# Performance work log

Hardware: AMD Instinct MI355X
Metric: run time of the kernel (lower is better)

## Reference

```python
import jax, jax.numpy as jnp
import numpy as np

H = 4096      # hidden_size
D = 1024      # mem_dim
A = 512       # attn_dim
B, LQ, TM = 4, 2048, 1500
EPS = 1e-5


def _layernorm(x, w, b):
    mu = jnp.mean(x, axis=-1, keepdims=True)
    var = jnp.var(x, axis=-1, keepdims=True)
    return (x - mu) * jax.lax.rsqrt(var + EPS) * w + b


def setup_inputs() -> dict:
    key = jax.random.key(0)
    ks = jax.random.split(key, 12)
    s = lambda fan_in: 1.0 / np.sqrt(fan_in)
    return {
        "hidden": jax.random.normal(ks[0], (B, LQ, H), jnp.float32),
        "mem": jax.random.normal(ks[1], (B, TM, D), jnp.float32),
        "mem_mask": jnp.zeros((B, TM), dtype=bool),
        "Wq": jax.random.uniform(ks[2], (H, A), jnp.float32, -s(H), s(H)),
        "bq": jnp.zeros((A,), jnp.float32),
        "Wk": jax.random.uniform(ks[3], (D, A), jnp.float32, -s(D), s(D)),
        "bk": jnp.zeros((A,), jnp.float32),
        "Wv": jax.random.uniform(ks[4], (D, A), jnp.float32, -s(D), s(D)),
        "bv": jnp.zeros((A,), jnp.float32),
        "Wo": jax.random.uniform(ks[5], (A, H), jnp.float32, -s(A), s(A)),
        "bo": jnp.zeros((H,), jnp.float32),
        "ln_in_w": jnp.ones((H,), jnp.float32),
        "ln_in_b": jnp.zeros((H,), jnp.float32),
        "ln_out_w": jnp.ones((H,), jnp.float32),
        "ln_out_b": jnp.zeros((H,), jnp.float32),
        "gate_logit": jnp.float32(-2.0),
    }


def reference(hidden, mem, mem_mask, Wq, bq, Wk, bk, Wv, bv, Wo, bo,
              ln_in_w, ln_in_b, ln_out_w, ln_out_b, gate_logit):
    h_norm = _layernorm(hidden, ln_in_w, ln_in_b)            # [B,LQ,H]
    Q = h_norm @ Wq + bq                                     # [B,LQ,A]
    K = mem @ Wk + bk                                        # [B,TM,A]
    V = mem @ Wv + bv                                        # [B,TM,A]
    scale = 1.0 / jnp.sqrt(jnp.float32(Q.shape[-1]))
    scores = jnp.einsum('bqa,bka->bqk', Q, K) * scale        # [B,LQ,TM]
    scores = jnp.where(mem_mask[:, None, :], jnp.float32(-1e30), scores)
    attn = jax.nn.softmax(scores, axis=-1)
    context = jnp.einsum('bqk,bka->bqa', attn, V)            # [B,LQ,A]
    context_h = context @ Wo + bo                            # [B,LQ,H]
    out_base = _layernorm(hidden + context_h, ln_out_w, ln_out_b)
    g = jax.nn.sigmoid(gate_logit)
    return hidden + g * (out_base - hidden)
```

## Files before the change

### kernel.cpp

```cpp
#include <hip/hip_runtime.h>
#include <cstdint>
#include <cstddef>

#define H_   4096
#define D_   1024
#define A_   512
#define B_   4
#define LQ_  2048
#define TM_  1500
#define TMP_ 1536
#define EPS_ 1e-5f

typedef __attribute__((ext_vector_type(8))) _Float16 half8;
typedef __attribute__((ext_vector_type(4))) _Float16 half4v;
typedef __attribute__((ext_vector_type(4))) float f32x4;

__device__ __forceinline__ void gload_lds16(void* g, void* l) {
  __builtin_amdgcn_global_load_lds((__attribute__((address_space(1))) void*)g,
                                   (__attribute__((address_space(3))) void*)l,
                                   16, 0, 0);
}

template <int OUTMODE>
__device__ __forceinline__ void gemm_tile(
    const _Float16* __restrict__ A, int lda,
    const _Float16* __restrict__ Bt, int ldb,
    const float* __restrict__ bias,
    void* __restrict__ C, int ldc,
    int Mvalid, int m0, int n0, int kbase, int kiters, float scale,
    _Float16* As, _Float16* Bs,
    const unsigned char* __restrict__ mrow, float* __restrict__ lsum, int nvalid) {
  const int tid = threadIdx.x;
  const int lane = tid & 63;
  const int wave = tid >> 6;

  f32x4 acc[4][4];
#pragma unroll
  for (int i = 0; i < 4; ++i)
#pragma unroll
    for (int jj = 0; jj < 4; ++jj) acc[i][jj] = (f32x4){0.f, 0.f, 0.f, 0.f};

  const _Float16* gA[2];
  const _Float16* gB[2];
  _Float16* lA[2];
  _Float16* lB[2];
#pragma unroll
  for (int i = 0; i < 2; ++i) {
    const int c = wave * 64 + lane + 256 * i;
    const int r = c >> 2;
    const int cs = c & 3;
    const int col = (cs ^ ((r >> 1) & 3)) * 8;
    int ra = m0 + r;
    if (ra >= Mvalid) ra = Mvalid - 1;
    gA[i] = A + (size_t)ra * lda + kbase + col;
    gB[i] = Bt + (size_t)(n0 + r) * ldb + kbase + col;
    lA[i] = As + wave * 512 + i * 2048;
    lB[i] = Bs + wave * 512 + i * 2048;
  }

  const int wm = (wave >> 1) * 64;
  const int wn = (wave & 1) * 64;
  const int rsub = lane & 15;
  const int j = lane >> 4;
  const int slot = j ^ ((rsub >> 1) & 3);

  for (int kt = 0; kt < kiters; ++kt) {
    const int ko = kt * 32;
#pragma unroll
    for (int i = 0; i < 2; ++i) {
      gload_lds16((void*)(gA[i] + ko), (void*)lA[i]);
      gload_lds16((void*)(gB[i] + ko), (void*)lB[i]);
    }
    __syncthreads();
    half8 af[4], bfr[4];
#pragma unroll
    for (int x = 0; x < 4; ++x) {
      af[x]  = *(const half8*)&As[(wm + x * 16 + rsub) * 32 + slot * 8];
      bfr[x] = *(const half8*)&Bs[(wn + x * 16 + rsub) * 32 + slot * 8];
    }
#pragma unroll
    for (int mi = 0; mi < 4; ++mi)
#pragma unroll
      for (int ni = 0; ni < 4; ++ni)
        acc[mi][ni] = __builtin_amdgcn_mfma_f32_16x16x32_f16(af[mi], bfr[ni], acc[mi][ni], 0, 0, 0);
    __syncthreads();
  }

  const int cn = n0 + wn + rsub;
  const int rm = m0 + wm + j * 4;

  if (OUTMODE == 3) {
    bool ok[4];
#pragma unroll
    for (int ni = 0; ni < 4; ++ni) {
      const int n = cn + ni * 16;
      const int nc = n < nvalid ? n : nvalid - 1;
      ok[ni] = (n < nvalid) && (mrow[nc] == 0);
    }
#pragma unroll
    for (int mi = 0; mi < 4; ++mi) {
#pragma unroll
      for (int r = 0; r < 4; ++r) {
        const int m = rm + mi * 16 + r;
        float rowsum = 0.f;
#pragma unroll
        for (int ni = 0; ni < 4; ++ni) {
          const int n = cn + ni * 16;
          const float e = ok[ni] ? __expf(acc[mi][ni][r] * scale) : 0.f;
          ((_Float16*)C)[(size_t)m * ldc + n] = (_Float16)e;
          rowsum += e;
        }
#pragma unroll
        for (int d = 1; d < 16; d <<= 1) rowsum += __shfl_xor(rowsum, d);
        if (rsub == 0) atomicAdd(&lsum[m], rowsum);
      }
    }
    return;
  }

  if (OUTMODE == 1) {
#pragma unroll
    for (int ni = 0; ni < 4; ++ni) {
      const int n = cn + ni * 16;
      const float bi = bias ? bias[n] : 0.f;
#pragma unroll
      for (int mi = 0; mi < 4; ++mi) {
        half4v pk;
#pragma unroll
        for (int r = 0; r < 4; ++r) pk[r] = (_Float16)(acc[mi][ni][r] * scale + bi);
        *(half4v*)&((_Float16*)C)[(size_t)n * ldc + rm + mi * 16] = pk;
      }
    }
    return;
  }

#pragma unroll
  for (int ni = 0; ni < 4; ++ni) {
    const int n = cn + ni * 16;
    const float bi = (OUTMODE == 0 && bias) ? bias[n] : 0.f;
#pragma unroll
    for (int mi = 0; mi < 4; ++mi) {
#pragma unroll
      for (int r = 0; r < 4; ++r) {
        const int m = rm + mi * 16 + r;
        const float v = acc[mi][ni][r] * scale + bi;
        if (OUTMODE == 0) ((_Float16*)C)[(size_t)m * ldc + n] = (_Float16)v;
        else ((float*)C)[(size_t)m * ldc + n] = v;
      }
    }
  }
}

template <int OUTMODE>
__global__ __launch_bounds__(256) void gemm_nt_kernel(
    const _Float16* __restrict__ Aall, size_t strideA, int lda,
    const _Float16* __restrict__ Btall, size_t strideB, int ldb,
    const float* __restrict__ bias,
    void* __restrict__ Call, size_t strideC, size_t strideS,
    int ldc, int Mvalid, int kiters, int nslices, int sliceK, float scale) {
  __shared__ __align__(16) _Float16 As[4096];
  __shared__ __align__(16) _Float16 Bs[4096];
  const int nx = gridDim.x, ny = gridDim.y;
  int id = (int)blockIdx.x + nx * ((int)blockIdx.y + ny * (int)blockIdx.z);
  const int tot = nx * ny * (int)gridDim.z;
  id = (id & 7) * (tot >> 3) + (id >> 3);
  const int bx = id % nx;
  const int by = (id / nx) % ny;
  const int bz = id / (nx * ny);
  const int batch = bz / nslices;
  const int slice = bz % nslices;
  const _Float16* A = Aall + (size_t)batch * strideA;
  const _Float16* Bt = Btall + (size_t)batch * strideB;
  char* C = (char*)Call + ((size_t)batch * strideC + (size_t)slice * strideS) *
                          (OUTMODE == 2 ? 4 : 2);
  gemm_tile<OUTMODE>(A, lda, Bt, ldb, bias, (void*)C, ldc, Mvalid,
                     by * 128, bx * 128, slice * sliceK, kiters,
                     scale, As, Bs, nullptr, nullptr, 0);
}

#define WO_NKH 16
__global__ __launch_bounds__(512, 1) void wo8_kernel(
    const _Float16* __restrict__ Ag,
    const _Float16* __restrict__ Bg,
    const float* __restrict__ bias,
    _Float16* __restrict__ Cg) {
  __shared__ __align__(16) _Float16 lds[65536];
  const int tid = threadIdx.x;
  const int lane = tid & 63;
  const int wave = tid >> 6;
  const int wr = wave >> 2;
  const int wc = wave & 3;
  int id = (int)blockIdx.x;
  id = (id & 7) * 64 + (id >> 3);
  const int by = id >> 4;
  const int bx = id & 15;
  const int m0 = by * 256, n0 = bx * 256;

  const _Float16* srcA[2];
  const _Float16* srcB[2];
  _Float16* dstA[2];
  _Float16* dstB[2];
#pragma unroll
  for (int p = 0; p < 2; ++p) {
    const int c = p * 512 + tid;
    const int r = c >> 2, cs = c & 3;
    const int col = (cs ^ ((r >> 1) & 3)) * 8;
    srcA[p] = Ag + (size_t)(m0 + r) * 512 + col;
    srcB[p] = Bg + (size_t)(n0 + r) * 512 + col;
    dstA[p] = lds + (p * 512 + wave * 64) * 8;
    dstB[p] = lds + 32768 + (p * 512 + wave * 64) * 8;
  }

  const int rsub = lane & 15;
  const int j = lane >> 4;
  const int sc_ = j ^ ((rsub >> 1) & 3);

  f32x4 acc[8][4];
#pragma unroll
  for (int i = 0; i < 8; ++i)
#pragma unroll
    for (int n = 0; n < 4; ++n) acc[i][n] = (f32x4){0.f, 0.f, 0.f, 0.f};

#pragma unroll
  for (int p = 0; p < 2; ++p) gload_lds16((void*)(srcA[p]), (void*)(dstA[p]));
#pragma unroll
  for (int p = 0; p < 2; ++p) gload_lds16((void*)(srcB[p]), (void*)(dstB[p]));
#pragma unroll
  for (int p = 0; p < 2; ++p) gload_lds16((void*)(srcA[p] + 32), (void*)(dstA[p] + 8192));
#pragma unroll
  for (int p = 0; p < 2; ++p) gload_lds16((void*)(srcB[p] + 32), (void*)(dstB[p] + 8192));
  asm volatile("s_waitcnt vmcnt(4)" ::: "memory");
  __builtin_amdgcn_s_barrier();

  half8 bf[4];
  for (int h = 0; h < WO_NKH; ++h) {
    const int sl = h & 3;
    const _Float16* Asl = lds + sl * 8192;
    const _Float16* Bsl = lds + 32768 + sl * 8192;
    if (h + 2 < WO_NKH) {
      const int s2 = (h + 2) & 3;
#pragma unroll
      for (int p = 0; p < 2; ++p)
        gload_lds16((void*)(srcA[p] + (h + 2) * 32), (void*)(dstA[p] + s2 * 8192));
    }
    half8 af[4];
#pragma unroll
    for (int x = 0; x < 4; ++x) {
      af[x] = *(const half8*)&Asl[(wr * 128 + x * 16 + rsub) * 32 + sc_ * 8];
      bf[x] = *(const half8*)&Bsl[(wc * 64 + x * 16 + rsub) * 32 + sc_ * 8];
    }
    __builtin_amdgcn_s_barrier();
    __builtin_amdgcn_s_setprio(1);
#pragma unroll
    for (int mi = 0; mi < 4; ++mi)
#pragma unroll
      for (int ni = 0; ni < 4; ++ni)
        acc[mi][ni] = __builtin_amdgcn_mfma_f32_16x16x32_f16(af[mi], bf[ni], acc[mi][ni], 0, 0, 0);
    __builtin_amdgcn_s_setprio(0);
    __builtin_amdgcn_s_barrier();
    if (h + 2 < WO_NKH) {
      const int s2 = (h + 2) & 3;
#pragma unroll
      for (int p = 0; p < 2; ++p)
        gload_lds16((void*)(srcB[p] + (h + 2) * 32), (void*)(dstB[p] + s2 * 8192));
    }
#pragma unroll
    for (int x = 0; x < 4; ++x)
      af[x] = *(const half8*)&Asl[(wr * 128 + 64 + x * 16 + rsub) * 32 + sc_ * 8];
    if (h < WO_NKH - 2) {
      asm volatile("s_waitcnt vmcnt(4)" ::: "memory");
    } else if (h == WO_NKH - 2) {
      asm volatile("s_waitcnt vmcnt(0)" ::: "memory");
    }
    __builtin_amdgcn_s_barrier();
    __builtin_amdgcn_s_setprio(1);
#pragma unroll
    for (int mi = 0; mi < 4; ++mi)
#pragma unroll
      for (int ni = 0; ni < 4; ++ni)
        acc[4 + mi][ni] = __builtin_amdgcn_mfma_f32_16x16x32_f16(af[mi], bf[ni], acc[4 + mi][ni], 0, 0, 0);
    __builtin_amdgcn_s_setprio(0);
    __builtin_amdgcn_s_barrier();
  }

  const int cn0 = n0 + wc * 64 + rsub;
  const int rm0 = m0 + wr * 128 + j * 4;
#pragma unroll
  for (int ni = 0; ni < 4; ++ni) {
    const int n = cn0 + ni * 16;
    const float bi = bias[n];
#pragma unroll
    for (int mh = 0; mh < 2; ++mh)
#pragma unroll
      for (int mi = 0; mi < 4; ++mi)
#pragma unroll
        for (int r = 0; r < 4; ++r) {
          const int m = rm0 + mh * 64 + mi * 16 + r;
          Cg[(size_t)m * 4096 + n] = (_Float16)(acc[mh * 4 + mi][ni][r] + bi);
        }
  }
}

__global__ __launch_bounds__(256) void scores_kernel(
    const _Float16* __restrict__ Qh, const _Float16* __restrict__ Kp,
    _Float16* __restrict__ sc, const unsigned char* __restrict__ mask,
    float* __restrict__ lsum) {
  __shared__ __align__(16) _Float16 As[4096];
  __shared__ __align__(16) _Float16 Bs[4096];
  const int nx = gridDim.x, ny = gridDim.y;
  int id = (int)blockIdx.x + nx * ((int)blockIdx.y + ny * (int)blockIdx.z);
  const int tot = nx * ny * (int)gridDim.z;
  id = (id & 7) * (tot >> 3) + (id >> 3);
  const int bx = id % nx;
  const int by = (id / nx) % ny;
  const int b = id / (nx * ny);
  gemm_tile<3>(Qh + (size_t)b * LQ_ * A_, A_, Kp + (size_t)b * TMP_ * A_, A_, nullptr,
               (void*)(sc + (size_t)b * LQ_ * TMP_), TMP_, LQ_,
               by * 128, bx * 128, 0, 16, 0.044194173824159216f,
               As, Bs, mask + (size_t)b * TM_, lsum + (size_t)b * LQ_, TM_);
}

__global__ __launch_bounds__(256) void qkv_kernel(
    const _Float16* __restrict__ hnorm, const _Float16* __restrict__ WqT,
    float* __restrict__ Qpart,
    const _Float16* __restrict__ memh, const _Float16* __restrict__ WkT,
    const float* __restrict__ bk, _Float16* __restrict__ Kp,
    const _Float16* __restrict__ WvT, const float* __restrict__ bv,
    _Float16* __restrict__ VT) {
  __shared__ __align__(16) _Float16 As[4096];
  __shared__ __align__(16) _Float16 Bs[4096];
  const int bid0 = blockIdx.x;
  if (bid0 < 512) {
    const int bid = ((bid0 & 7) << 6) | (bid0 >> 3);
    const int nb = bid & 3, mb = (bid >> 2) & 63, ks = bid >> 8;
    gemm_tile<2>(hnorm, H_, WqT, H_, nullptr,
                 (void*)(Qpart + (size_t)ks * 8192 * A_), A_,
                 8192, mb * 128, nb * 128, ks * 2048, 64, 1.f, As, Bs,
                 nullptr, nullptr, 0);
  } else if (bid0 < 704) {
    int t = bid0 - 512;
    t = (t & 7) * 24 + (t >> 3);
    const int nb = t & 3, mb = (t >> 2) % 12, b = t / 48;
    gemm_tile<0>(memh + (size_t)b * TM_ * D_, D_, WkT, D_, bk,
                 (void*)(Kp + (size_t)b * TMP_ * A_), A_,
                 TM_, mb * 128, nb * 128, 0, 32, 1.f, As, Bs,
                 nullptr, nullptr, 0);
  } else {
    int t = bid0 - 704;
    t = (t & 7) * 24 + (t >> 3);
    const int nb = t & 3, mb = (t >> 2) % 12, b = t / 48;
    gemm_tile<1>(memh + (size_t)b * TM_ * D_, D_, WvT, D_, bv,
                 (void*)(VT + (size_t)b * A_ * TMP_), TMP_,
                 TM_, mb * 128, nb * 128, 0, 32, 1.f, As, Bs,
                 nullptr, nullptr, 0);
  }
}

__global__ __launch_bounds__(256) void qreduce_kernel(
    const float* __restrict__ p, const float* __restrict__ bias,
    _Float16* __restrict__ out, float* __restrict__ lsum) {
  const int bid = blockIdx.x;
  if (bid >= 4096) {
    lsum[(bid - 4096) * 256 + threadIdx.x] = 0.f;
    return;
  }
  const size_t i = ((size_t)bid * 256 + threadIdx.x) * 4;
  const float4 a = *(const float4*)(p + i);
  const float4 b = *(const float4*)(p + (size_t)8192 * A_ + i);
  const float4 bi = *(const float4*)(bias + (i & (A_ - 1)));
  half4v o;
  o.x = (_Float16)(a.x + b.x + bi.x);
  o.y = (_Float16)(a.y + b.y + bi.y);
  o.z = (_Float16)(a.z + b.z + bi.z);
  o.w = (_Float16)(a.w + b.w + bi.w);
  *(half4v*)(out + i) = o;
}

__global__ __launch_bounds__(256) void areduce_kernel(
    const float* __restrict__ p, const float* __restrict__ lsum,
    _Float16* __restrict__ out) {
  const size_t S = (size_t)B_ * LQ_ * A_;
  const size_t i = ((size_t)blockIdx.x * 256 + threadIdx.x) * 4;
  const float4 a = *(const float4*)(p + i);
  const float4 b = *(const float4*)(p + S + i);
  const float4 c = *(const float4*)(p + 2 * S + i);
  const float inv = 1.f / lsum[i >> 9];
  half4v o;
  o.x = (_Float16)((a.x + b.x + c.x) * inv);
  o.y = (_Float16)((a.y + b.y + c.y) * inv);
  o.z = (_Float16)((a.z + b.z + c.z) * inv);
  o.w = (_Float16)((a.w + b.w + c.w) * inv);
  *(half4v*)(out + i) = o;
}

__global__ __launch_bounds__(256) void ln1_kernel(
    const float* __restrict__ hidden, const float* __restrict__ lnw,
    const float* __restrict__ lnb, _Float16* __restrict__ hnorm) {
  const int t = threadIdx.x;
  const int lane = t & 63;
  const int row = blockIdx.x * 4 + (t >> 6);
  const float* x = hidden + (size_t)row * H_;
  _Float16* y = hnorm + (size_t)row * H_;
  float4 v[16];
  float s = 0.f, ss = 0.f;
#pragma unroll
  for (int i = 0; i < 16; ++i) {
    v[i] = ((const float4*)x)[lane + 64 * i];
    s  += v[i].x + v[i].y + v[i].z + v[i].w;
    ss += v[i].x * v[i].x + v[i].y * v[i].y + v[i].z * v[i].z + v[i].w * v[i].w;
  }
#pragma unroll
  for (int off = 32; off; off >>= 1) { s += __shfl_xor(s, off); ss += __shfl_xor(ss, off); }
  const float mu = s * (1.f / H_);
  const float var = ss * (1.f / H_) - mu * mu;
  const float rstd = rsqrtf(var + EPS_);
#pragma unroll
  for (int i = 0; i < 16; ++i) {
    float4 wv4 = ((const float4*)lnw)[lane + 64 * i];
    float4 bv4 = ((const float4*)lnb)[lane + 64 * i];
    half4v o;
    o.x = (_Float16)((v[i].x - mu) * rstd * wv4.x + bv4.x);
    o.y = (_Float16)((v[i].y - mu) * rstd * wv4.y + bv4.y);
    o.z = (_Float16)((v[i].z - mu) * rstd * wv4.z + bv4.z);
    o.w = (_Float16)((v[i].w - mu) * rstd * wv4.w + bv4.w);
    ((half4v*)y)[lane + 64 * i] = o;
  }
}

__global__ __launch_bounds__(256) void misc_kernel(
    const float* __restrict__ mem, _Float16* __restrict__ memh,
    const float* __restrict__ Wq, _Float16* __restrict__ WqT,
    const float* __restrict__ Wk, _Float16* __restrict__ WkT,
    const float* __restrict__ Wv, _Float16* __restrict__ WvT,
    const float* __restrict__ Wo, _Float16* __restrict__ WoT) {
  __shared__ float smem[32 * 33];
  int bid = blockIdx.x;
  const int t = threadIdx.x;
  if (bid < 1500) {
    const size_t i = ((size_t)bid * 256 + t) * 4;
    float4 f = *(const float4*)(mem + i);
    half4v o;
    o.x = (_Float16)f.x; o.y = (_Float16)f.y; o.z = (_Float16)f.z; o.w = (_Float16)f.w;
    *(half4v*)(memh + i) = o;
    return;
  }
  bid -= 1500;
  const float* src;
  _Float16* dst;
  int R, C;
  if (bid < 2048) { src = Wq; dst = WqT; R = 4096; C = 512; }
  else if (bid < 2048 + 512) { bid -= 2048; src = Wk; dst = WkT; R = 1024; C = 512; }
  else if (bid < 2048 + 1024) { bid -= 2048 + 512; src = Wv; dst = WvT; R = 1024; C = 512; }
  else { bid -= 2048 + 1024; src = Wo; dst = WoT; R = 512; C = 4096; }
  const int nbx = C / 32;
  const int bx = bid % nbx, by = bid / nbx;
  const int tx = t & 31, ty = t >> 5;
  const int c0 = bx * 32, r0 = by * 32;
#pragma unroll
  for (int i = 0; i < 32; i += 8)
    smem[(ty + i) * 33 + tx] = src[(size_t)(r0 + ty + i) * C + c0 + tx];
  __syncthreads();
  {
    const int q = t & 7, cc = t >> 3;
    half4v g;
#pragma unroll
    for (int e = 0; e < 4; ++e) g[e] = (_Float16)smem[(4 * q + e) * 33 + cc];
    *(half4v*)&dst[(size_t)(c0 + cc) * R + r0 + 4 * q] = g;
  }
}

__global__ __launch_bounds__(256) void ln2_gate_kernel(
    const float* __restrict__ hidden_, const _Float16* __restrict__ ctxh_,
    const float* __restrict__ w, const float* __restrict__ bvec,
    const float* __restrict__ gate_logit, float* __restrict__ out_) {
  const int row = blockIdx.x;
  const float* h = hidden_ + (size_t)row * H_;
  const _Float16* c = ctxh_ + (size_t)row * H_;
  float* o = out_ + (size_t)row * H_;
  const int t = threadIdx.x;
  float4 hv[4];
  float xv[16];
  float s = 0.f, ss = 0.f;
#pragma unroll
  for (int i = 0; i < 4; ++i) {
    hv[i] = ((const float4*)h)[t + 256 * i];
    half4v cv = ((const half4v*)c)[t + 256 * i];
    xv[4 * i + 0] = hv[i].x + (float)cv.x;
    xv[4 * i + 1] = hv[i].y + (float)cv.y;
    xv[4 * i + 2] = hv[i].z + (float)cv.z;
    xv[4 * i + 3] = hv[i].w + (float)cv.w;
    s  += xv[4 * i + 0] + xv[4 * i + 1] + xv[4 * i + 2] + xv[4 * i + 3];
    ss += xv[4 * i + 0] * xv[4 * i + 0] + xv[4 * i + 1] * xv[4 * i + 1] +
          xv[4 * i + 2] * xv[4 * i + 2] + xv[4 * i + 3] * xv[4 * i + 3];
  }
  __shared__ float red[2][4];
  const int lane = t & 63, wv = t >> 6;
#pragma unroll
  for (int off = 32; off; off >>= 1) { s += __shfl_down(s, off); ss += __shfl_down(ss, off); }
  if (lane == 0) { red[0][wv] = s; red[1][wv] = ss; }
  __syncthreads();
  s  = red[0][0] + red[0][1] + red[0][2] + red[0][3];
  ss = red[1][0] + red[1][1] + red[1][2] + red[1][3];
  const float mu = s * (1.f / H_);
  const float var = ss * (1.f / H_) - mu * mu;
  const float rstd = rsqrtf(var + EPS_);
  const float g = 1.f / (1.f + __expf(-gate_logit[0]));
#pragma unroll
  for (int i = 0; i < 4; ++i) {
    float4 wv4 = ((const float4*)w)[t + 256 * i];
    float4 bv4 = ((const float4*)bvec)[t + 256 * i];
    float4 ov;
    ov.x = hv[i].x + g * ((xv[4 * i + 0] - mu) * rstd * wv4.x + bv4.x - hv[i].x);
    ov.y = hv[i].y + g * ((xv[4 * i + 1] - mu) * rstd * wv4.y + bv4.y - hv[i].y);
    ov.z = hv[i].z + g * ((xv[4 * i + 2] - mu) * rstd * wv4.z + bv4.z - hv[i].z);
    ov.w = hv[i].w + g * ((xv[4 * i + 3] - mu) * rstd * wv4.w + bv4.w - hv[i].w);
    ((float4*)o)[t + 256 * i] = ov;
  }
}

extern "C" void kernel_launch(void* const* d_in, const int* in_sizes, int n_in,
                              void* d_out, int out_size, void* d_ws, size_t ws_size,
                              hipStream_t stream) {
  const float* hidden = (const float*)d_in[0];
  const float* mem    = (const float*)d_in[1];
  const unsigned char* mask = (const unsigned char*)d_in[2];
  const float* Wq = (const float*)d_in[3];
  const float* bq = (const float*)d_in[4];
  const float* Wk = (const float*)d_in[5];
  const float* bk = (const float*)d_in[6];
  const float* Wv = (const float*)d_in[7];
  const float* bv = (const float*)d_in[8];
  const float* Wo = (const float*)d_in[9];
  const float* bo = (const float*)d_in[10];
  const float* lnw1 = (const float*)d_in[11];
  const float* lnb1 = (const float*)d_in[12];
  const float* lnw2 = (const float*)d_in[13];
  const float* lnb2 = (const float*)d_in[14];
  const float* gate = (const float*)d_in[15];
  float* out = (float*)d_out;

  _Float16* p = (_Float16*)d_ws;
  _Float16* hnorm = p; p += (size_t)8192 * H_;
  _Float16* Qh    = p; p += (size_t)8192 * A_;
  _Float16* memh  = p; p += (size_t)6000 * D_;
  _Float16* WqT   = p; p += (size_t)A_ * H_;
  _Float16* WkT   = p; p += (size_t)A_ * D_;
  _Float16* WvT   = p; p += (size_t)A_ * D_;
  _Float16* WoT   = p; p += (size_t)H_ * A_;
  _Float16* Kp    = p; p += (size_t)B_ * TMP_ * A_;
  _Float16* VT    = p; p += (size_t)B_ * A_ * TMP_;
  _Float16* sc    = p; p += (size_t)B_ * LQ_ * TMP_;
  _Float16* ctx   = p; p += (size_t)8192 * A_;
  float* Qpart = (float*)sc;
  float* Apart = (float*)hnorm;
  float* lsum  = (float*)WkT;

  ln1_kernel<<<2048, 256, 0, stream>>>(hidden, lnw1, lnb1, hnorm);
  misc_kernel<<<1500 + 2048 + 512 + 512 + 2048, 256, 0, stream>>>(
      mem, memh, Wq, WqT, Wk, WkT, Wv, WvT, Wo, WoT);
  qkv_kernel<<<896, 256, 0, stream>>>(hnorm, WqT, Qpart, memh, WkT, bk, Kp, WvT, bv, VT);
  qreduce_kernel<<<4096 + 32, 256, 0, stream>>>(Qpart, bq, Qh, lsum);
  scores_kernel<<<dim3(12, 16, 4), 256, 0, stream>>>(Qh, Kp, sc, mask, lsum);
  gemm_nt_kernel<2><<<dim3(4, 16, 12), 256, 0, stream>>>(
      sc, (size_t)LQ_ * TMP_, TMP_, VT, (size_t)A_ * TMP_, TMP_, nullptr,
      (void*)Apart, (size_t)LQ_ * A_, (size_t)B_ * LQ_ * A_, A_, LQ_, 16, 3, 512, 1.f);
  areduce_kernel<<<4096, 256, 0, stream>>>(Apart, lsum, ctx);
  wo8_kernel<<<512, 512, 0, stream>>>(ctx, WoT, bo, hnorm);
  ln2_gate_kernel<<<8192, 256, 0, stream>>>(hidden, hnorm, lnw2, lnb2, gate, out);
}
```

Baseline: 511.4 us.

## Generalize 256x256 MFMA tile and use it for Q projection and PV GEMMs

Turns the pipelined 256x256 Wo GEMM body into a reusable device tile with configurable strides, K offset and output mode. The Q projection (split-K 4) and the attention-value GEMM (split-K 3) now use this larger tile in place of the 128x128 gemm_tile, which should raise data reuse per block. Q projection is split out of the combined qkv kernel into its own launch, and the Q partial buffer grows to four slices in a separate workspace region instead of aliasing the scores buffer. The trade-offs are fewer blocks (256 and 192) on a large GPU, more split-K partial traffic for Q, and one extra launch.

```diff
diff --git a/kernel.cpp b/kernel.cpp
--- a/kernel.cpp
+++ b/kernel.cpp
@@ -152,49 +152,17 @@
 }
 
 template <int OUTMODE>
-__global__ __launch_bounds__(256) void gemm_nt_kernel(
-    const _Float16* __restrict__ Aall, size_t strideA, int lda,
-    const _Float16* __restrict__ Btall, size_t strideB, int ldb,
+__device__ __forceinline__ void mfma256_tile(
+    const _Float16* __restrict__ Ag, int lda,
+    const _Float16* __restrict__ Bg, int ldb,
     const float* __restrict__ bias,
-    void* __restrict__ Call, size_t strideC, size_t strideS,
-    int ldc, int Mvalid, int kiters, int nslices, int sliceK, float scale) {
-  __shared__ __align__(16) _Float16 As[4096];
-  __shared__ __align__(16) _Float16 Bs[4096];
-  const int nx = gridDim.x, ny = gridDim.y;
-  int id = (int)blockIdx.x + nx * ((int)blockIdx.y + ny * (int)blockIdx.z);
-  const int tot = nx * ny * (int)gridDim.z;
-  id = (id & 7) * (tot >> 3) + (id >> 3);
-  const int bx = id % nx;
-  const int by = (id / nx) % ny;
-  const int bz = id / (nx * ny);
-  const int batch = bz / nslices;
-  const int slice = bz % nslices;
-  const _Float16* A = Aall + (size_t)batch * strideA;
-  const _Float16* Bt = Btall + (size_t)batch * strideB;
-  char* C = (char*)Call + ((size_t)batch * strideC + (size_t)slice * strideS) *
-                          (OUTMODE == 2 ? 4 : 2);
-  gemm_tile<OUTMODE>(A, lda, Bt, ldb, bias, (void*)C, ldc, Mvalid,
-                     by * 128, bx * 128, slice * sliceK, kiters,
-                     scale, As, Bs, nullptr, nullptr, 0);
-}
-
-#define WO_NKH 16
-__global__ __launch_bounds__(512, 1) void wo8_kernel(
-    const _Float16* __restrict__ Ag,
-    const _Float16* __restrict__ Bg,
-    const float* __restrict__ bias,
-    _Float16* __restrict__ Cg) {
-  __shared__ __align__(16) _Float16 lds[65536];
+    void* __restrict__ Cg, int ldc,
+    int m0, int n0, int kbase, int nkh, _Float16* lds) {
   const int tid = threadIdx.x;
   const int lane = tid & 63;
   const int wave = tid >> 6;
   const int wr = wave >> 2;
   const int wc = wave & 3;
-  int id = (int)blockIdx.x;
-  id = (id & 7) * 64 + (id >> 3);
-  const int by = id >> 4;
-  const int bx = id & 15;
-  const int m0 = by * 256, n0 = bx * 256;
 
   const _Float16* srcA[2];
   const _Float16* srcB[2];
@@ -205,8 +173,8 @@
     const int c = p * 512 + tid;
     const int r = c >> 2, cs = c & 3;
     const int col = (cs ^ ((r >> 1) & 3)) * 8;
-    srcA[p] = Ag + (size_t)(m0 + r) * 512 + col;
-    srcB[p] = Bg + (size_t)(n0 + r) * 512 + col;
+    srcA[p] = Ag + (size_t)(m0 + r) * lda + kbase + col;
+    srcB[p] = Bg + (size_t)(n0 + r) * ldb + kbase + col;
     dstA[p] = lds + (p * 512 + wave * 64) * 8;
     dstB[p] = lds + 32768 + (p * 512 + wave * 64) * 8;
   }
@@ -233,11 +201,11 @@
   __builtin_amdgcn_s_barrier();
 
   half8 bf[4];
-  for (int h = 0; h < WO_NKH; ++h) {
+  for (int h = 0; h < nkh; ++h) {
     const int sl = h & 3;
     const _Float16* Asl = lds + sl * 8192;
     const _Float16* Bsl = lds + 32768 + sl * 8192;
-    if (h + 2 < WO_NKH) {
+    if (h + 2 < nkh) {
       const int s2 = (h + 2) & 3;
 #pragma unroll
       for (int p = 0; p < 2; ++p)
@@ -258,7 +226,7 @@
         acc[mi][ni] = __builtin_amdgcn_mfma_f32_16x16x32_f16(af[mi], bf[ni], acc[mi][ni], 0, 0, 0);
     __builtin_amdgcn_s_setprio(0);
     __builtin_amdgcn_s_barrier();
-    if (h + 2 < WO_NKH) {
+    if (h + 2 < nkh) {
       const int s2 = (h + 2) & 3;
 #pragma unroll
       for (int p = 0; p < 2; ++p)
@@ -267,9 +235,9 @@
 #pragma unroll
     for (int x = 0; x < 4; ++x)
       af[x] = *(const half8*)&Asl[(wr * 128 + 64 + x * 16 + rsub) * 32 + sc_ * 8];
-    if (h < WO_NKH - 2) {
+    if (h < nkh - 2) {
       asm volatile("s_waitcnt vmcnt(4)" ::: "memory");
-    } else if (h == WO_NKH - 2) {
+    } else if (h == nkh - 2) {
       asm volatile("s_waitcnt vmcnt(0)" ::: "memory");
     }
     __builtin_amdgcn_s_barrier();
@@ -288,7 +256,7 @@
 #pragma unroll
   for (int ni = 0; ni < 4; ++ni) {
     const int n = cn0 + ni * 16;
-    const float bi = bias[n];
+    const float bi = (OUTMODE == 0) ? bias[n] : 0.f;
 #pragma unroll
     for (int mh = 0; mh < 2; ++mh)
 #pragma unroll
@@ -296,9 +264,54 @@
 #pragma unroll
         for (int r = 0; r < 4; ++r) {
           const int m = rm0 + mh * 64 + mi * 16 + r;
-          Cg[(size_t)m * 4096 + n] = (_Float16)(acc[mh * 4 + mi][ni][r] + bi);
+          if (OUTMODE == 0)
+            ((_Float16*)Cg)[(size_t)m * ldc + n] = (_Float16)(acc[mh * 4 + mi][ni][r] + bi);
+          else
+            ((float*)Cg)[(size_t)m * ldc + n] = acc[mh * 4 + mi][ni][r];
         }
   }
+}
+
+__global__ __launch_bounds__(512, 1) void wo8_kernel(
+    const _Float16* __restrict__ Ag, const _Float16* __restrict__ Bg,
+    const float* __restrict__ bias, _Float16* __restrict__ Cg) {
+  __shared__ __align__(16) _Float16 lds[65536];
+  int id = (int)blockIdx.x;
+  id = (id & 7) * 64 + (id >> 3);
+  const int by = id >> 4, bx = id & 15;
+  mfma256_tile<0>(Ag, 512, Bg, 512, bias, (void*)Cg, 4096,
+                  by * 256, bx * 256, 0, 16, lds);
+}
+
+__global__ __launch_bounds__(512, 1) void q8_kernel(
+    const _Float16* __restrict__ hnorm, const _Float16* __restrict__ WqT,
+    float* __restrict__ Qpart4) {
+  __shared__ __align__(16) _Float16 lds[65536];
+  int id = (int)blockIdx.x;
+  id = (id & 7) * 32 + (id >> 3);
+  const int slice = id >> 6;
+  const int t2 = id & 63;
+  const int by = t2 >> 1, bx = t2 & 1;
+  mfma256_tile<2>(hnorm, 4096, WqT, 4096, nullptr,
+                  (void*)(Qpart4 + (size_t)slice * 8192 * A_), A_,
+                  by * 256, bx * 256, slice * 1024, 32, lds);
+}
+
+__global__ __launch_bounds__(512, 1) void pv8_kernel(
+    const _Float16* __restrict__ sc, const _Float16* __restrict__ VT,
+    float* __restrict__ Apart) {
+  __shared__ __align__(16) _Float16 lds[65536];
+  int id = (int)blockIdx.x;
+  id = (id & 7) * 24 + (id >> 3);
+  const int b = id / 48;
+  const int rem = id % 48;
+  const int slice = rem / 16;
+  const int tile = rem % 16;
+  const int by = tile >> 1, bx = tile & 1;
+  mfma256_tile<2>(sc + (size_t)b * LQ_ * TMP_, TMP_,
+                  VT + (size_t)b * A_ * TMP_, TMP_, nullptr,
+                  (void*)(Apart + (size_t)slice * B_ * LQ_ * A_ + (size_t)b * LQ_ * A_), A_,
+                  by * 256, bx * 256, slice * 512, 16, lds);
 }
 
 __global__ __launch_bounds__(256) void scores_kernel(
@@ -320,9 +333,7 @@
                As, Bs, mask + (size_t)b * TM_, lsum + (size_t)b * LQ_, TM_);
 }
 
-__global__ __launch_bounds__(256) void qkv_kernel(
-    const _Float16* __restrict__ hnorm, const _Float16* __restrict__ WqT,
-    float* __restrict__ Qpart,
+__global__ __launch_bounds__(256) void kv_kernel(
     const _Float16* __restrict__ memh, const _Float16* __restrict__ WkT,
     const float* __restrict__ bk, _Float16* __restrict__ Kp,
     const _Float16* __restrict__ WvT, const float* __restrict__ bv,
@@ -330,15 +341,8 @@
   __shared__ __align__(16) _Float16 As[4096];
   __shared__ __align__(16) _Float16 Bs[4096];
   const int bid0 = blockIdx.x;
-  if (bid0 < 512) {
-    const int bid = ((bid0 & 7) << 6) | (bid0 >> 3);
-    const int nb = bid & 3, mb = (bid >> 2) & 63, ks = bid >> 8;
-    gemm_tile<2>(hnorm, H_, WqT, H_, nullptr,
-                 (void*)(Qpart + (size_t)ks * 8192 * A_), A_,
-                 8192, mb * 128, nb * 128, ks * 2048, 64, 1.f, As, Bs,
-                 nullptr, nullptr, 0);
-  } else if (bid0 < 704) {
-    int t = bid0 - 512;
+  if (bid0 < 192) {
+    int t = bid0;
     t = (t & 7) * 24 + (t >> 3);
     const int nb = t & 3, mb = (t >> 2) % 12, b = t / 48;
     gemm_tile<0>(memh + (size_t)b * TM_ * D_, D_, WkT, D_, bk,
@@ -346,7 +350,7 @@
                  TM_, mb * 128, nb * 128, 0, 32, 1.f, As, Bs,
                  nullptr, nullptr, 0);
   } else {
-    int t = bid0 - 704;
+    int t = bid0 - 192;
     t = (t & 7) * 24 + (t >> 3);
     const int nb = t & 3, mb = (t >> 2) % 12, b = t / 48;
     gemm_tile<1>(memh + (size_t)b * TM_ * D_, D_, WvT, D_, bv,
@@ -364,15 +368,18 @@
     lsum[(bid - 4096) * 256 + threadIdx.x] = 0.f;
     return;
   }
+  const size_t S2 = (size_t)8192 * A_;
   const size_t i = ((size_t)bid * 256 + threadIdx.x) * 4;
   const float4 a = *(const float4*)(p + i);
-  const float4 b = *(const float4*)(p + (size_t)8192 * A_ + i);
+  const float4 b = *(const float4*)(p + S2 + i);
+  const float4 c = *(const float4*)(p + 2 * S2 + i);
+  const float4 d = *(const float4*)(p + 3 * S2 + i);
   const float4 bi = *(const float4*)(bias + (i & (A_ - 1)));
   half4v o;
-  o.x = (_Float16)(a.x + b.x + bi.x);
-  o.y = (_Float16)(a.y + b.y + bi.y);
-  o.z = (_Float16)(a.z + b.z + bi.z);
-  o.w = (_Float16)(a.w + b.w + bi.w);
+  o.x = (_Float16)(a.x + b.x + c.x + d.x + bi.x);
+  o.y = (_Float16)(a.y + b.y + c.y + d.y + bi.y);
+  o.z = (_Float16)(a.z + b.z + c.z + d.z + bi.z);
+  o.w = (_Float16)(a.w + b.w + c.w + d.w + bi.w);
   *(half4v*)(out + i) = o;
 }
 
@@ -551,19 +558,18 @@
   _Float16* VT    = p; p += (size_t)B_ * A_ * TMP_;
   _Float16* sc    = p; p += (size_t)B_ * LQ_ * TMP_;
   _Float16* ctx   = p; p += (size_t)8192 * A_;
-  float* Qpart = (float*)sc;
+  float* Qpart4   = (float*)p; p += (size_t)4 * 8192 * A_ * 2;
   float* Apart = (float*)hnorm;
   float* lsum  = (float*)WkT;
 
   ln1_kernel<<<2048, 256, 0, stream>>>(hidden, lnw1, lnb1, hnorm);
   misc_kernel<<<1500 + 2048 + 512 + 512 + 2048, 256, 0, stream>>>(
       mem, memh, Wq, WqT, Wk, WkT, Wv, WvT, Wo, WoT);
-  qkv_kernel<<<896, 256, 0, stream>>>(hnorm, WqT, Qpart, memh, WkT, bk, Kp, WvT, bv, VT);
-  qreduce_kernel<<<4096 + 32, 256, 0, stream>>>(Qpart, bq, Qh, lsum);
+  q8_kernel<<<256, 512, 0, stream>>>(hnorm, WqT, Qpart4);
+  kv_kernel<<<384, 256, 0, stream>>>(memh, WkT, bk, Kp, WvT, bv, VT);
+  qreduce_kernel<<<4096 + 32, 256, 0, stream>>>(Qpart4, bq, Qh, lsum);
   scores_kernel<<<dim3(12, 16, 4), 256, 0, stream>>>(Qh, Kp, sc, mask, lsum);
-  gemm_nt_kernel<2><<<dim3(4, 16, 12), 256, 0, stream>>>(
-      sc, (size_t)LQ_ * TMP_, TMP_, VT, (size_t)A_ * TMP_, TMP_, nullptr,
-      (void*)Apart, (size_t)LQ_ * A_, (size_t)B_ * LQ_ * A_, A_, LQ_, 16, 3, 512, 1.f);
+  pv8_kernel<<<192, 512, 0, stream>>>(sc, VT, Apart);
   areduce_kernel<<<4096, 256, 0, stream>>>(Apart, lsum, ctx);
   wo8_kernel<<<512, 512, 0, stream>>>(ctx, WoT, bo, hnorm);
   ln2_gate_kernel<<<8192, 256, 0, stream>>>(hidden, hnorm, lnw2, lnb2, gate, out);
```

Measured after the change: 521.4 us. About the same (+2.0%).
